# Optimization experiments

Measured on AMD Instinct MI355X. Metric: run time of the kernel, lower is better.

Reference implementation:

```python
import math
import jax, jax.numpy as jnp
import numpy as np

SAMPLE_RATE = 24000
HARMONIC_NUM = 8
SINE_AMP = 0.1


def setup_inputs() -> dict:
    key = jax.random.key(0)
    k1, k2, k3 = jax.random.split(key, 3)
    f0 = jax.random.uniform(k1, (32, 800), dtype=jnp.float32)  # frame-rate F0
    W = jax.random.normal(k2, (9, 1), dtype=jnp.float32) * (1.0 / 3.0)  # Linear(9,1) weight
    b = jax.random.normal(k3, (1,), dtype=jnp.float32) * 0.01
    return {"f0": f0, "W": W, "b": b, "upp": 240}


def reference(f0, W, b, upp):
    # nearest-neighbor upsample by integer factor upp == repeat each frame
    f0_up = jnp.repeat(f0, upp, axis=1)  # [batch, samples]
    batch, samples = f0_up.shape
    # harmonic multipliers h = 1..harmonic_num+1 (9 harmonics)
    h = jnp.arange(1, HARMONIC_NUM + 2, dtype=f0.dtype)  # [9]
    # cumsum(f0_up * h) == cumsum(f0_up) * h (cumsum is linear); one scan for all harmonics
    base_phase = jnp.cumsum(f0_up / SAMPLE_RATE, axis=1)  # [batch, samples]
    phase = base_phase[:, :, None] * (h * (2.0 * math.pi))  # [batch, samples, 9]
    sine = jnp.sin(phase) * SINE_AMP
    uv = (f0_up > 0).astype(f0.dtype)[:, :, None]  # [batch, samples, 1]
    harmonics = sine * uv
    har_source = jnp.tanh(harmonics @ W + b)  # [batch, samples, 1]
    noise = jax.random.normal(jax.random.key(1234), (batch, samples, 1), dtype=f0.dtype) * (SINE_AMP / 3.0)
    return (har_source, noise, uv)
```

## Files before the change

### kernel.cpp

```cpp
#include <hip/hip_runtime.h>
#include <stdint.h>

#define FRAMES  800
#define UPP     240
#define SAMPLES (FRAMES * UPP)
#define BATCH   32
#define NTOT    (BATCH * SAMPLES)
#define SPT     8
#define BLK     256
#define SPB     (BLK * SPT)
#define NFRM    10

__device__ __forceinline__ uint32_t rotl32(uint32_t v, int d) {
  return (v << d) | (v >> (32 - d));
}

__device__ __forceinline__ void threefry2x32(uint32_t k0, uint32_t k1,
                                             uint32_t x0, uint32_t x1,
                                             uint32_t& o0, uint32_t& o1) {
  const uint32_t ks0 = k0, ks1 = k1, ks2 = k0 ^ k1 ^ 0x1BD11BDAu;
  x0 += ks0; x1 += ks1;
#define TF_R(r) { x0 += x1; x1 = rotl32(x1, r); x1 ^= x0; }
  TF_R(13) TF_R(15) TF_R(26) TF_R(6)   x0 += ks1; x1 += ks2 + 1u;
  TF_R(17) TF_R(29) TF_R(16) TF_R(24)  x0 += ks2; x1 += ks0 + 2u;
  TF_R(13) TF_R(15) TF_R(26) TF_R(6)   x0 += ks0; x1 += ks1 + 3u;
  TF_R(17) TF_R(29) TF_R(16) TF_R(24)  x0 += ks1; x1 += ks2 + 4u;
  TF_R(13) TF_R(15) TF_R(26) TF_R(6)   x0 += ks2; x1 += ks0 + 5u;
#undef TF_R
  o0 = x0; o1 = x1;
}

__device__ __forceinline__ float erfinv_f32(float x) {
  float q  = __fmul_rn(x, x);
  float om = __fsub_rn(1.0f, q);
  float w  = -0.69314718f * __builtin_amdgcn_logf(om);

  float wm = w - 2.5f;
  float pm = 2.81022636e-08f;
  pm = fmaf(pm, wm, 3.43273939e-07f);
  pm = fmaf(pm, wm, -3.5233877e-06f);
  pm = fmaf(pm, wm, -4.39150654e-06f);
  pm = fmaf(pm, wm, 0.00021858087f);
  pm = fmaf(pm, wm, -0.00125372503f);
  pm = fmaf(pm, wm, -0.00417768164f);
  pm = fmaf(pm, wm, 0.246640727f);
  pm = fmaf(pm, wm, 1.50140941f);

  float wt = __builtin_amdgcn_sqrtf(w) - 3.0f;
  float pt = -0.000200214257f;
  pt = fmaf(pt, wt, 0.000100950558f);
  pt = fmaf(pt, wt, 0.00134934322f);
  pt = fmaf(pt, wt, -0.00367342844f);
  pt = fmaf(pt, wt, 0.00573950773f);
  pt = fmaf(pt, wt, -0.0076224613f);
  pt = fmaf(pt, wt, 0.00943887047f);
  pt = fmaf(pt, wt, 1.00167406f);
  pt = fmaf(pt, wt, 2.83297682f);

  float p = (w < 5.0f) ? pm : pt;
  return p * x;
}

__device__ __forceinline__ float bits_to_noise(uint32_t bits) {
  float f = __uint_as_float((bits >> 9) | 0x3f800000u);
  float u = f - 1.0f;
  const float lo = -0.99999994f;
  float val = fmaf(u, 2.0f, lo);
  val = fmaxf(lo, val);
  float n = 1.41421356f * erfinv_f32(val);
  return n * 0.033333335f;
}

__device__ __forceinline__ float fast_tanhf(float x) {
  float e = __expf(-2.0f * x);
  return (1.0f - e) * __builtin_amdgcn_rcpf(1.0f + e);
}

__global__ __launch_bounds__(256) void fused_kernel(
    const float* __restrict__ f0, const float* __restrict__ W,
    const float* __restrict__ bptr, float* __restrict__ out) {
  const int row = blockIdx.y;
  const float* f0row = f0 + row * FRAMES;
  const int blockSample0 = blockIdx.x * SPB;
  const int Fb = blockSample0 / UPP;
  const int tid = (int)threadIdx.x;

  __shared__ double sPart[4];
  __shared__ float  sPre[NFRM];

  double p = 0.0;
  for (int i = tid; i < Fb; i += BLK) p += (double)f0row[i];
#pragma unroll
  for (int off = 32; off > 0; off >>= 1) p += __shfl_xor(p, off, 64);
  if ((tid & 63) == 0) sPart[tid >> 6] = p;
  __syncthreads();

  if (tid < NFRM) {
    double base = (sPart[0] + sPart[1]) + (sPart[2] + sPart[3]);
    for (int i = 0; i < tid; ++i) {
      int idx = Fb + i;
      idx = (idx < FRAMES) ? idx : (FRAMES - 1);
      base += (double)f0row[idx];
    }
    double c = base * 0.01;
    sPre[tid] = (float)(c - floor(c));
  }
  __syncthreads();

  const int t0 = blockSample0 + tid * SPT;
  if (t0 >= SAMPLES) return;

  const int frame = t0 / UPP;
  const float pf = sPre[frame - Fb];
  const int j = t0 - frame * UPP;
  const float fv   = f0row[frame];
  const float step = fv * (1.0f / 24000.0f);
  const float amp  = (fv > 0.0f) ? 0.1f : 0.0f;
  const float uvf  = (fv > 0.0f) ? 1.0f : 0.0f;

  float Wr[9];
#pragma unroll
  for (int h = 0; h < 9; ++h) Wr[h] = W[h];
  const float bias = bptr[0];

  const uint32_t gbase = (uint32_t)(row * SAMPLES + t0);

  float hq[SPT], nq[SPT];

#pragma unroll
  for (int k = 0; k < SPT; ++k) {
    float ph = fmaf((float)(j + 1 + k), step, pf);
    ph = __builtin_amdgcn_fractf(ph);
    float s1 = __builtin_amdgcn_sinf(ph);
    float c1 = __builtin_amdgcn_cosf(ph);
    float tc = 2.0f * c1;
    float skm1 = 0.0f, sk = s1;
    float dot = Wr[0] * s1;
#pragma unroll
    for (int h = 2; h <= 9; ++h) {
      float sn = fmaf(tc, sk, -skm1);
      skm1 = sk; sk = sn;
      dot = fmaf(Wr[h - 1], sn, dot);
    }
    hq[k] = fast_tanhf(fmaf(amp, dot, bias));
  }

#pragma unroll
  for (int k = 0; k < SPT; ++k) {
    uint32_t a, b;
    threefry2x32(0u, 1234u, 0u, gbase + (uint32_t)k, a, b);
    nq[k] = bits_to_noise(a ^ b);
  }

  float* har   = out;
  float* noise = out + NTOT;
  float* uvp   = out + 2 * NTOT;
  *(float4*)(har + gbase)       = make_float4(hq[0], hq[1], hq[2], hq[3]);
  *(float4*)(har + gbase + 4)   = make_float4(hq[4], hq[5], hq[6], hq[7]);
  *(float4*)(noise + gbase)     = make_float4(nq[0], nq[1], nq[2], nq[3]);
  *(float4*)(noise + gbase + 4) = make_float4(nq[4], nq[5], nq[6], nq[7]);
  const float4 uv4 = make_float4(uvf, uvf, uvf, uvf);
  *(float4*)(uvp + gbase)       = uv4;
  *(float4*)(uvp + gbase + 4)   = uv4;
}

extern "C" void kernel_launch(void* const* d_in, const int* in_sizes, int n_in,
                              void* d_out, int out_size, void* d_ws, size_t ws_size,
                              hipStream_t stream) {
  const float* f0 = (const float*)d_in[0];
  const float* W  = (const float*)d_in[1];
  const float* b  = (const float*)d_in[2];
  (void)d_ws; (void)ws_size;

  float* out = (float*)d_out;
  dim3 g((SAMPLES + SPB - 1) / SPB, BATCH);
  fused_kernel<<<g, BLK, 0, stream>>>(f0, W, b, out);
}
```

Baseline: 102.6 us.

## Pack sine and noise math into paired float2 ops and rotate phases

Rewrites the per-thread harmonic and noise computation to work on two samples at once using float2 vector types, so the compiler can emit packed FMA instructions (v_pk_fma_f32 on CDNA). Instead of one sin/cos per sample, it evaluates sin/cos once at the first phase and advances by angle-addition rotation. It also replaces the exp-based tanh with an odd polynomial, which is only accurate for small arguments. These trade transcendental and scalar ALU work for packed FMAs, at the cost of accumulated rotation error and the tanh approximation being valid only for the bounded harmonic sum.

```diff
diff --git a/kernel.cpp b/kernel.cpp
--- a/kernel.cpp
+++ b/kernel.cpp
@@ -10,6 +10,24 @@
 #define BLK     256
 #define SPB     (BLK * SPT)
 #define NFRM    10
+
+typedef float v2f __attribute__((ext_vector_type(2)));
+
+#if __has_builtin(__builtin_elementwise_fma)
+#define VFMA(a, b, c) __builtin_elementwise_fma((a), (b), (c))
+#else
+#define VFMA(a, b, c) ((a) * (b) + (c))
+#endif
+
+__device__ __forceinline__ v2f vset(float a, float b) { v2f r; r.x = a; r.y = b; return r; }
+__device__ __forceinline__ v2f vsplat(float a) { v2f r; r.x = a; r.y = a; return r; }
+__device__ __forceinline__ v2f vmax(v2f a, v2f b) {
+#if __has_builtin(__builtin_elementwise_max)
+  return __builtin_elementwise_max(a, b);
+#else
+  return vset(fmaxf(a.x, b.x), fmaxf(a.y, b.y));
+#endif
+}
 
 __device__ __forceinline__ uint32_t rotl32(uint32_t v, int d) {
   return (v << d) | (v >> (32 - d));
@@ -30,50 +48,68 @@
   o0 = x0; o1 = x1;
 }
 
-__device__ __forceinline__ float erfinv_f32(float x) {
-  float q  = __fmul_rn(x, x);
-  float om = __fsub_rn(1.0f, q);
-  float w  = -0.69314718f * __builtin_amdgcn_logf(om);
-
-  float wm = w - 2.5f;
-  float pm = 2.81022636e-08f;
-  pm = fmaf(pm, wm, 3.43273939e-07f);
-  pm = fmaf(pm, wm, -3.5233877e-06f);
-  pm = fmaf(pm, wm, -4.39150654e-06f);
-  pm = fmaf(pm, wm, 0.00021858087f);
-  pm = fmaf(pm, wm, -0.00125372503f);
-  pm = fmaf(pm, wm, -0.00417768164f);
-  pm = fmaf(pm, wm, 0.246640727f);
-  pm = fmaf(pm, wm, 1.50140941f);
-
-  float wt = __builtin_amdgcn_sqrtf(w) - 3.0f;
-  float pt = -0.000200214257f;
-  pt = fmaf(pt, wt, 0.000100950558f);
-  pt = fmaf(pt, wt, 0.00134934322f);
-  pt = fmaf(pt, wt, -0.00367342844f);
-  pt = fmaf(pt, wt, 0.00573950773f);
-  pt = fmaf(pt, wt, -0.0076224613f);
-  pt = fmaf(pt, wt, 0.00943887047f);
-  pt = fmaf(pt, wt, 1.00167406f);
-  pt = fmaf(pt, wt, 2.83297682f);
-
-  float p = (w < 5.0f) ? pm : pt;
-  return p * x;
-}
-
-__device__ __forceinline__ float bits_to_noise(uint32_t bits) {
-  float f = __uint_as_float((bits >> 9) | 0x3f800000u);
-  float u = f - 1.0f;
-  const float lo = -0.99999994f;
-  float val = fmaf(u, 2.0f, lo);
-  val = fmaxf(lo, val);
-  float n = 1.41421356f * erfinv_f32(val);
-  return n * 0.033333335f;
-}
-
-__device__ __forceinline__ float fast_tanhf(float x) {
-  float e = __expf(-2.0f * x);
-  return (1.0f - e) * __builtin_amdgcn_rcpf(1.0f + e);
+__device__ __forceinline__ v2f noise_pair(uint32_t b0, uint32_t b1) {
+  v2f F = vset(__uint_as_float((b0 >> 9) | 0x3f800000u),
+               __uint_as_float((b1 >> 9) | 0x3f800000u));
+  v2f val = VFMA(F, vsplat(2.0f), vsplat(-2.99999994f));
+  val = vmax(val, vsplat(-0.99999994f));
+  v2f xs = val * vsplat(0.04714045f);
+  v2f q  = val * val;
+  v2f om = vsplat(1.0f) - q;
+  v2f w;
+  w.x = -0.69314718f * __builtin_amdgcn_logf(om.x);
+  w.y = -0.69314718f * __builtin_amdgcn_logf(om.y);
+
+  v2f wm = w - vsplat(2.5f);
+  v2f pm = vsplat(2.81022636e-08f);
+  pm = VFMA(pm, wm, vsplat(3.43273939e-07f));
+  pm = VFMA(pm, wm, vsplat(-3.5233877e-06f));
+  pm = VFMA(pm, wm, vsplat(-4.39150654e-06f));
+  pm = VFMA(pm, wm, vsplat(0.00021858087f));
+  pm = VFMA(pm, wm, vsplat(-0.00125372503f));
+  pm = VFMA(pm, wm, vsplat(-0.00417768164f));
+  pm = VFMA(pm, wm, vsplat(0.246640727f));
+  pm = VFMA(pm, wm, vsplat(1.50140941f));
+
+  v2f wt;
+  wt.x = __builtin_amdgcn_sqrtf(w.x) - 3.0f;
+  wt.y = __builtin_amdgcn_sqrtf(w.y) - 3.0f;
+  v2f pt = vsplat(-0.000200214257f);
+  pt = VFMA(pt, wt, vsplat(0.000100950558f));
+  pt = VFMA(pt, wt, vsplat(0.00134934322f));
+  pt = VFMA(pt, wt, vsplat(-0.00367342844f));
+  pt = VFMA(pt, wt, vsplat(0.00573950773f));
+  pt = VFMA(pt, wt, vsplat(-0.0076224613f));
+  pt = VFMA(pt, wt, vsplat(0.00943887047f));
+  pt = VFMA(pt, wt, vsplat(1.00167406f));
+  pt = VFMA(pt, wt, vsplat(2.83297682f));
+
+  v2f p;
+  p.x = (w.x < 5.0f) ? pm.x : pt.x;
+  p.y = (w.y < 5.0f) ? pm.y : pt.y;
+  return p * xs;
+}
+
+__device__ __forceinline__ v2f har_pair(v2f S, v2f C, const float* Wr,
+                                        float amp, float bias) {
+  v2f tc = C + C;
+  v2f skm1 = vsplat(0.0f);
+  v2f sk = S;
+  v2f dot = vsplat(Wr[0]) * S;
+#pragma unroll
+  for (int h = 2; h <= 9; ++h) {
+    v2f sn = VFMA(tc, sk, -skm1);
+    skm1 = sk; sk = sn;
+    dot = VFMA(vsplat(Wr[h - 1]), sn, dot);
+  }
+  v2f x = VFMA(vsplat(amp), dot, vsplat(bias));
+  v2f t = x * x;
+  v2f pp = vsplat(0.021869489f);
+  pp = VFMA(pp, t, vsplat(-0.053968254f));
+  pp = VFMA(pp, t, vsplat(0.13333333f));
+  pp = VFMA(pp, t, vsplat(-0.33333333f));
+  pp = VFMA(pp, t, vsplat(1.0f));
+  return x * pp;
 }
 
 __global__ __launch_bounds__(256) void fused_kernel(
@@ -125,40 +161,48 @@
 
   const uint32_t gbase = (uint32_t)(row * SAMPLES + t0);
 
-  float hq[SPT], nq[SPT];
-
-#pragma unroll
-  for (int k = 0; k < SPT; ++k) {
-    float ph = fmaf((float)(j + 1 + k), step, pf);
-    ph = __builtin_amdgcn_fractf(ph);
-    float s1 = __builtin_amdgcn_sinf(ph);
-    float c1 = __builtin_amdgcn_cosf(ph);
-    float tc = 2.0f * c1;
-    float skm1 = 0.0f, sk = s1;
-    float dot = Wr[0] * s1;
-#pragma unroll
-    for (int h = 2; h <= 9; ++h) {
-      float sn = fmaf(tc, sk, -skm1);
-      skm1 = sk; sk = sn;
-      dot = fmaf(Wr[h - 1], sn, dot);
-    }
-    hq[k] = fast_tanhf(fmaf(amp, dot, bias));
-  }
-
+  uint32_t r[SPT];
 #pragma unroll
   for (int k = 0; k < SPT; ++k) {
     uint32_t a, b;
     threefry2x32(0u, 1234u, 0u, gbase + (uint32_t)k, a, b);
-    nq[k] = bits_to_noise(a ^ b);
+    r[k] = a ^ b;
   }
+  v2f n01 = noise_pair(r[0], r[1]);
+  v2f n23 = noise_pair(r[2], r[3]);
+  v2f n45 = noise_pair(r[4], r[5]);
+  v2f n67 = noise_pair(r[6], r[7]);
+
+  const float ph0 = fmaf((float)(j + 1), step, pf);
+  const float s0 = __builtin_amdgcn_sinf(ph0);
+  const float c0 = __builtin_amdgcn_cosf(ph0);
+  const float ss = __builtin_amdgcn_sinf(step);
+  const float cs = __builtin_amdgcn_cosf(step);
+  const float s1 = fmaf(s0, cs, c0 * ss);
+  const float c1 = fmaf(c0, cs, -(s0 * ss));
+  const float s2 = 2.0f * ss * cs;
+  const float c2 = fmaf(-2.0f * ss, ss, 1.0f);
+  const v2f s2v = vsplat(s2), c2v = vsplat(c2);
+
+  v2f S = vset(s0, s1), C = vset(c0, c1);
+  v2f h01 = har_pair(S, C, Wr, amp, bias);
+  v2f Sn = VFMA(S, c2v, C * s2v);
+  v2f Cn = VFMA(C, c2v, -(S * s2v));
+  v2f h23 = har_pair(Sn, Cn, Wr, amp, bias);
+  S = VFMA(Sn, c2v, Cn * s2v);
+  C = VFMA(Cn, c2v, -(Sn * s2v));
+  v2f h45 = har_pair(S, C, Wr, amp, bias);
+  Sn = VFMA(S, c2v, C * s2v);
+  Cn = VFMA(C, c2v, -(S * s2v));
+  v2f h67 = har_pair(Sn, Cn, Wr, amp, bias);
 
   float* har   = out;
   float* noise = out + NTOT;
   float* uvp   = out + 2 * NTOT;
-  *(float4*)(har + gbase)       = make_float4(hq[0], hq[1], hq[2], hq[3]);
-  *(float4*)(har + gbase + 4)   = make_float4(hq[4], hq[5], hq[6], hq[7]);
-  *(float4*)(noise + gbase)     = make_float4(nq[0], nq[1], nq[2], nq[3]);
-  *(float4*)(noise + gbase + 4) = make_float4(nq[4], nq[5], nq[6], nq[7]);
+  *(float4*)(har + gbase)       = make_float4(h01.x, h01.y, h23.x, h23.y);
+  *(float4*)(har + gbase + 4)   = make_float4(h45.x, h45.y, h67.x, h67.y);
+  *(float4*)(noise + gbase)     = make_float4(n01.x, n01.y, n23.x, n23.y);
+  *(float4*)(noise + gbase + 4) = make_float4(n45.x, n45.y, n67.x, n67.y);
   const float4 uv4 = make_float4(uvf, uvf, uvf, uvf);
   *(float4*)(uvp + gbase)       = uv4;
   *(float4*)(uvp + gbase + 4)   = uv4;
```

Measured after the change: 100.5 us. 2.0% less time.
